# Performance work log

Hardware: AMD Instinct MI355X
Metric: run time of the kernel (lower is better)

Reference implementation:

```python
import jax, jax.numpy as jnp
import numpy as np

NX, NY, C = 784, 480, 32
N0 = NX * NY          # 376320 level-0 nodes
N1 = N0 // 4          # 94080
N2 = N0 // 16         # 23520


def _gcn(x, w, b, ei, n):
    """PyG GCNConv: add self loops, symmetric norm, linear, scatter-sum, bias."""
    loop = jnp.arange(n, dtype=ei.dtype)
    src = jnp.concatenate([ei[0], loop])
    dst = jnp.concatenate([ei[1], loop])
    deg = jax.ops.segment_sum(jnp.ones(src.shape[0], x.dtype), dst, num_segments=n)
    dinv = jnp.where(deg > 0, jax.lax.rsqrt(deg), 0.0)
    norm = (dinv[src] * dinv[dst])[:, None]          # [E+n, 1]
    msg = (x @ w)[src] * norm                        # gather + scale
    return jax.ops.segment_sum(msg, dst, num_segments=n) + b


def _up2(x, h, w):
    """2x nearest-neighbor upsample of a row-major-flattened (h, w, C) grid."""
    g = x.reshape(h, w, x.shape[-1])
    return jnp.repeat(jnp.repeat(g, 2, axis=0), 2, axis=1).reshape(-1, x.shape[-1])


def setup_inputs() -> dict:
    key = jax.random.key(0)
    ks = jax.random.split(key, 20)
    f32 = jnp.float32
    inp = {
        "x": jax.random.normal(ks[0], (N0, 4), f32),
        "fc1_w": jax.random.normal(ks[1], (4, C), f32) * 0.1,
        "fc1_b": jax.random.normal(ks[2], (C,), f32) * 0.1,
        "w1": jax.random.normal(ks[3], (C, C), f32) * 0.1,
        "b1": jax.random.normal(ks[4], (C,), f32) * 0.1,
        "w2": jax.random.normal(ks[5], (C, C), f32) * 0.1,
        "b2": jax.random.normal(ks[6], (C,), f32) * 0.1,
        "w3": jax.random.normal(ks[7], (C, C), f32) * 0.1,
        "b3": jax.random.normal(ks[8], (C,), f32) * 0.1,
        "w4": jax.random.normal(ks[9], (C, C), f32) * 0.1,
        "b4": jax.random.normal(ks[10], (C,), f32) * 0.1,
        "w5": jax.random.normal(ks[11], (C, C), f32) * 0.1,
        "b5": jax.random.normal(ks[12], (C,), f32) * 0.1,
        "fc2_w": jax.random.normal(ks[13], (C, 3), f32) * 0.1,
        "fc2_b": jax.random.normal(ks[14], (3,), f32) * 0.1,
        "idx0": jnp.arange(N0, dtype=jnp.int32),
        "idx1": jnp.arange(N1, dtype=jnp.int32),
        "idx2": jnp.arange(N2, dtype=jnp.int32),
        "ei0": jax.random.randint(ks[15], (2, 4 * N0), 0, N0, dtype=jnp.int32),
        "ei1": jax.random.randint(ks[16], (2, 4 * N1), 0, N1, dtype=jnp.int32),
        "ei2": jax.random.randint(ks[17], (2, 4 * N2), 0, N2, dtype=jnp.int32),
    }
    return inp


def reference(x, fc1_w, fc1_b, w1, b1, w2, b2, w3, b3, w4, b4, w5, b5,
              fc2_w, fc2_b, idx0, idx1, idx2, ei0, ei1, ei2):
    h = jax.nn.relu(x @ fc1_w + fc1_b)                                  # [N0, 32]
    h = h.at[idx0].set(_gcn(h[idx0], w1, b1, ei0, idx0.shape[0]))
    h = jax.nn.relu(h)
    # level-1 downsample: take every other grid row/col
    h1 = h.reshape(NX, NY, C)[::2, ::2].reshape(-1, C)                  # [N1, 32]
    h1 = h1.at[idx1].set(_gcn(h1[idx1], w2, b2, ei1, idx1.shape[0]))
    h1 = jax.nn.relu(h1)
    # level-2 downsample
    h2 = h1.reshape(NX // 2, NY // 2, C)[::2, ::2].reshape(-1, C)       # [N2, 32]
    h2 = h2.at[idx2].set(_gcn(h2[idx2], w3, b3, ei2, idx2.shape[0]))
    h2 = jax.nn.relu(h2)
    # upsample level-2 -> level-1, residual add
    h1u = h1 + _up2(h2, NX // 4, NY // 4)
    h1u = h1u.at[idx1].set(_gcn(h1u[idx1], w4, b4, ei1, idx1.shape[0]))
    h1u = jax.nn.relu(h1u)
    # upsample level-1 -> level-0, residual add
    hu = h + _up2(h1u, NX // 2, NY // 2)
    hu = hu.at[idx0].set(_gcn(hu[idx0], w5, b5, ei0, idx0.shape[0]))
    hu = jax.nn.relu(hu)
    return (hu @ fc2_w + fc2_b)[idx0]                                   # [N0, 3]
```

## Files before the change

### kernel.cpp

```cpp
#include <hip/hip_runtime.h>
#include <hip/hip_bf16.h>

typedef unsigned short u16;
typedef unsigned int u32;
typedef float fx2 __attribute__((ext_vector_type(2)));

#define NXg 784
#define NYg 480
constexpr int N0c = NXg * NYg;
constexpr int N1c = N0c / 4;
constexpr int N2c = N0c / 16;
constexpr int NTc = N0c + N1c + N2c;
constexpr int E0c = 4 * N0c;
constexpr int E1c = 4 * N1c;
constexpr int E2c = 4 * N2c;
constexpr int NB0 = (N0c + 511) / 512;
constexpr int NB1 = (N1c + 511) / 512;
constexpr int NB2 = (N2c + 511) / 512;
constexpr int NBt = NB0 + NB1 + NB2;
constexpr int ECAP = 2560;
constexpr int CCAP = 4096;
constexpr int CHUNK = 8192;
constexpr int NC0 = (E0c + CHUNK - 1) / CHUNK;
constexpr int NC1 = (E1c + CHUNK - 1) / CHUNK;
constexpr int NC2 = (E2c + CHUNK - 1) / CHUNK;
constexpr int NCt = NC0 + NC1 + NC2;

__device__ __forceinline__ float bf2f(u16 v) {
    union { u32 u; float f; } t; t.u = ((u32)v) << 16; return t.f;
}
__device__ __forceinline__ u16 f2bf(float f) {
    union { float f; u32 u; } t; t.f = f;
    u32 u = t.u;
    u32 r = (u + 0x7fffu + ((u >> 16) & 1u)) >> 16;
    return (u16)r;
}
__device__ __forceinline__ float rdf(const void* p, int i, int isf32) {
    if (isf32) return ((const float*)p)[i];
    return bf2f(((const u16*)p)[i]);
}
__device__ __forceinline__ void stage(float* dst, const void* src, int n, int isf32) {
    int t = threadIdx.x;
    if (isf32) {
        const float* s = (const float*)src;
        for (int i = t; i < n; i += 256) dst[i] = s[i];
    } else {
        const u16* s = (const u16*)src;
        for (int i = t; i < n; i += 256) dst[i] = bf2f(s[i]);
    }
}

struct BF16S {
    typedef u16 T;
    static __device__ __forceinline__ float ld(const T* p, size_t i) { return bf2f(p[i]); }
    static __device__ __forceinline__ void st(T* p, size_t i, float v) { p[i] = f2bf(v); }
    static __device__ __forceinline__ fx2 ld2(const T* p, size_t i) {
        u32 w = ((const u32*)p)[i];
        fx2 r; r.x = bf2f((u16)(w & 0xffffu)); r.y = bf2f((u16)(w >> 16));
        return r;
    }
    static __device__ __forceinline__ void st2nt(T* p, size_t i, fx2 v) {
        u32 w = (u32)f2bf(v.x) | ((u32)f2bf(v.y) << 16);
        __builtin_nontemporal_store(w, (u32*)p + i);
    }
};

__device__ __forceinline__ void lvl_of_bin(int b, int& lv, int& bl) {
    if (b < NB0) { lv = 0; bl = b; }
    else if (b < NB0 + NB1) { lv = 1; bl = b - NB0; }
    else { lv = 2; bl = b - NB0 - NB1; }
}

__global__ void k_dinit(const u32* __restrict__ xw, int* __restrict__ flag,
                        int* __restrict__ binCursor, u16* __restrict__ y0,
                        u16* __restrict__ y1, u16* __restrict__ y2) {
    __shared__ int cnt;
    int t = threadIdx.x;
    int g = blockIdx.x * 256 + t;
    if (blockIdx.x == 0) {
        if (t == 0) cnt = 0;
        __syncthreads();
        u32 w = xw[t];
        int e = (int)((w >> 7) & 0xFFu);
        int hit = ((e >= 90 && e <= 135) || ((w & 0x7FFFu) == 0u)) ? 1 : 0;
        atomicAdd(&cnt, hit);
        __syncthreads();
        if (t == 0) *flag = (cnt < 192) ? 1 : 0;
    }
    if (g < NBt) binCursor[g] = g * ECAP;
    if (blockIdx.x == 1 && t < 32) { y0[t] = 0; y1[t] = 0; y2[t] = 0; }
}

__global__ void kC_place(const int* __restrict__ ei0, const int* __restrict__ ei1,
                         const int* __restrict__ ei2, int* __restrict__ binCursor,
                         u32* __restrict__ BE) {
    __shared__ int lc[NB0];
    __shared__ int lb[NB0];
    int b = blockIdx.x, t = threadIdx.x;
    int lv, cl;
    if (b < NC0) { lv = 0; cl = b; }
    else if (b < NC0 + NC1) { lv = 1; cl = b - NC0; }
    else { lv = 2; cl = b - NC0 - NC1; }
    const int* srcp; const int* dstp; int E, nb, binB;
    if (lv == 0) { srcp = ei0; dstp = ei0 + E0c; E = E0c; nb = NB0; binB = 0; }
    else if (lv == 1) { srcp = ei1; dstp = ei1 + E1c; E = E1c; nb = NB1; binB = NB0; }
    else { srcp = ei2; dstp = ei2 + E2c; E = E2c; nb = NB2; binB = NB0 + NB1; }
    for (int i = t; i < nb; i += 1024) lc[i] = 0;
    __syncthreads();
    int e0 = cl * CHUNK, e1 = min(E, e0 + CHUNK);
    for (int i = e0 + t; i < e1; i += 1024) atomicAdd(&lc[dstp[i] >> 9], 1);
    __syncthreads();
    for (int i = t; i < nb; i += 1024) {
        int c = lc[i];
        lb[i] = c ? atomicAdd(&binCursor[binB + i], c) : 0;
        lc[i] = 0;
    }
    __syncthreads();
    for (int i = e0 + t; i < e1; i += 1024) {
        int d = dstp[i];
        int bn = d >> 9;
        int p = atomicAdd(&lc[bn], 1);
        BE[lb[bn] + p] = ((u32)srcp[i] << 9) | (u32)(d & 511);
    }
}

__global__ void kD_all(const u32* __restrict__ BE, const int* __restrict__ binCursor,
                       float* __restrict__ DINV, u32* __restrict__ RPC,
                       int* __restrict__ colAll) {
    __shared__ int lc[512];
    __shared__ int lst[512];
    __shared__ int lcur[512];
    __shared__ int red[256];
    int b = blockIdx.x, t = threadIdx.x;
    int lv, bl; lvl_of_bin(b, lv, bl);
    int cbase, nLev, dummy;
    if (lv == 0) { cbase = 0; nLev = N0c; dummy = N0c; }
    else if (lv == 1) { cbase = N0c; nLev = N1c; dummy = N1c; }
    else { cbase = N0c + N1c; nLev = N2c; dummy = N2c; }
    lc[t] = 0; lc[t + 256] = 0;
    __syncthreads();
    int s0 = b * ECAP, s1 = binCursor[b];
    for (int i = s0 + t; i < s1; i += 256) atomicAdd(&lc[BE[i] & 511u], 1);
    __syncthreads();
    int nodeB = bl << 9;
    int pc[2];
    int ps = 0;
#pragma unroll
    for (int j = 0; j < 2; j++) {
        int li = t * 2 + j;
        int node = nodeB + li;
        int c = (node < nLev) ? lc[li] : 0;
        pc[j] = (c + 3) & ~3;
        ps += pc[j];
    }
    red[t] = ps;
    __syncthreads();
    for (int off = 1; off < 256; off <<= 1) {
        int x = (t >= off) ? red[t - off] : 0;
        __syncthreads();
        red[t] += x;
        __syncthreads();
    }
    int ex = red[t] - ps;
    int tot = red[255];
    int cb = b * CCAP;
    int off = ex;
#pragma unroll
    for (int j = 0; j < 2; j++) {
        int li = t * 2 + j;
        lst[li] = off;
        lcur[li] = off;
        off += pc[j];
    }
    __syncthreads();
#pragma unroll
    for (int j = 0; j < 2; j++) {
        int li = t * 2 + j;
        int node = nodeB + li;
        if (node < nLev) {
            int c = lc[li];
            DINV[cbase + node] = rsqrtf((float)c + 1.0f);
            int rp = cb + lst[li];
            u32 nch = (u32)((c + 3) >> 2);
            RPC[cbase + node] = ((u32)(rp >> 2) << 10) | nch;
        }
    }
    for (int i = t; i < tot; i += 256) colAll[cb + i] = dummy;
    __syncthreads();
    for (int i = s0 + t; i < s1; i += 256) {
        u32 e = BE[i];
        int p = atomicAdd(&lcur[e & 511u], 1);
        colAll[cb + p] = (int)(e >> 9);
    }
}

__device__ __forceinline__ fx2 gather2(const u16* __restrict__ ys,
                                       const u32* __restrict__ rpc,
                                       const int* __restrict__ col,
                                       const float* __restrict__ dinv,
                                       int node, int cp) {
    u32 v = rpc[node];
    int s0 = (int)((v >> 10) << 2);
    int nch = (int)(v & 1023u);
    fx2 a = BF16S::ld2(ys, (size_t)node * 16 + cp);
    const int4* c4 = (const int4*)(col + s0);
    for (int i = 0; i < nch; i++) {
        int4 cs = c4[i];
        fx2 a0 = BF16S::ld2(ys, (size_t)cs.x * 16 + cp);
        fx2 a1 = BF16S::ld2(ys, (size_t)cs.y * 16 + cp);
        fx2 a2 = BF16S::ld2(ys, (size_t)cs.z * 16 + cp);
        fx2 a3 = BF16S::ld2(ys, (size_t)cs.w * 16 + cp);
        a += (a0 + a1) + (a2 + a3);
    }
    float di = dinv[node];
    a *= di;
    return a;
}

constexpr int FC1_TILES = N0c / 64;
__global__ void k_fc1prep(const void* __restrict__ x, const void* __restrict__ fw,
                          const void* __restrict__ fb, const void* __restrict__ w1,
                          const float* __restrict__ d0, u16* __restrict__ ys1,
                          const int* __restrict__ flag) {
    int isf32 = *flag;
    __shared__ float sx[256];
    __shared__ float sh[64 * 33];
    __shared__ float sfw[128];
    __shared__ float sfb[32];
    __shared__ float sw1[1024];
    int t = threadIdx.x;
    stage(sw1, w1, 1024, isf32);
    stage(sfw, fw, 128, isf32);
    stage(sfb, fb, 32, isf32);
    __syncthreads();
    int c = t & 31;
    int ng = t >> 5;
    int ci0 = t & 15;
    int rgrp = t >> 4;
    for (int tile = blockIdx.x; tile < FC1_TILES; tile += gridDim.x) {
        int nodeBase = tile * 64;
        sx[t] = rdf(x, nodeBase * 4 + t, isf32);
        __syncthreads();
#pragma unroll
        for (int i = 0; i < 8; i++) {
            int ln = ng + i * 8;
            float a = sfb[c];
#pragma unroll
            for (int k = 0; k < 4; k++) a = fmaf(sx[ln * 4 + k], sfw[k * 32 + c], a);
            sh[ln * 33 + c] = fmaxf(a, 0.0f);
        }
        __syncthreads();
        float acc[4][2];
#pragma unroll
        for (int r = 0; r < 4; r++) { acc[r][0] = 0.0f; acc[r][1] = 0.0f; }
#pragma unroll
        for (int k = 0; k < 32; k++) {
            float w0 = sw1[k * 32 + ci0];
            float w1v = sw1[k * 32 + ci0 + 16];
#pragma unroll
            for (int r = 0; r < 4; r++) {
                float s = sh[(rgrp * 4 + r) * 33 + k];
                acc[r][0] = fmaf(s, w0, acc[r][0]);
                acc[r][1] = fmaf(s, w1v, acc[r][1]);
            }
        }
#pragma unroll
        for (int r = 0; r < 4; r++) {
            int node = nodeBase + rgrp * 4 + r;
            float dv = d0[node];
            BF16S::st(ys1, (size_t)node * 32 + ci0, acc[r][0] * dv);
            BF16S::st(ys1, (size_t)node * 32 + ci0 + 16, acc[r][1] * dv);
        }
        __syncthreads();
    }
}

template <int NPB>
__global__ void k_gds(const u16* __restrict__ ys_in, const u32* __restrict__ rpc,
                      const int* __restrict__ col,
                      const float* __restrict__ dinv_p, const void* __restrict__ b,
                      u16* __restrict__ O, const void* __restrict__ wn,
                      const float* __restrict__ dinv_c, u16* __restrict__ ys_out,
                      int cols, const int* __restrict__ flag) {
    int isf32 = *flag;
    __shared__ float sv[NPB * 32];
    __shared__ float swn[1024];
    int t = threadIdx.x;
    int nodeBase = blockIdx.x * NPB;
    int rb = nodeBase / cols;
    if (!(rb & 1)) stage(swn, wn, 1024, isf32);
    int cp = t & 15;
#pragma unroll
    for (int i = 0; i < NPB / 16; i++) {
        int local = (t >> 4) + i * 16;
        int node = nodeBase + local;
        fx2 g = gather2(ys_in, rpc, col, dinv_p, node, cp);
        fx2 v;
        v.x = fmaxf(g.x + rdf(b, 2 * cp, isf32), 0.0f);
        v.y = fmaxf(g.y + rdf(b, 2 * cp + 1, isf32), 0.0f);
        BF16S::st2nt(O, (size_t)node * 16 + cp, v);
        sv[local * 32 + 2 * cp] = v.x;
        sv[local * 32 + 2 * cp + 1] = v.y;
    }
    __syncthreads();
    if (!(rb & 1)) {
#pragma unroll
        for (int i = 0; i < NPB / 16; i++) {
            int item = t + i * 256;
            int childIdx = item >> 5;
            int ci = item & 31;
            int lc = childIdx * 2;
            int cc = (nodeBase - rb * cols) + lc;
            int dn = (rb >> 1) * (cols >> 1) + (cc >> 1);
            float a = 0.0f;
#pragma unroll
            for (int k = 0; k < 32; k++) a = fmaf(sv[lc * 32 + k], swn[k * 32 + ci], a);
            BF16S::st(ys_out, (size_t)dn * 32 + ci, a * dinv_c[dn]);
        }
    }
}

template <int NPB>
__global__ void k_gup(const u16* __restrict__ ys_in, const u32* __restrict__ rpc,
                      const int* __restrict__ col,
                      const float* __restrict__ dinv_p, const void* __restrict__ b,
                      const u16* __restrict__ R, const void* __restrict__ wn,
                      const float* __restrict__ dinv_c, u16* __restrict__ ys_out,
                      int cols_p, const int* __restrict__ flag) {
    constexpr int RPT = NPB / 4;
    int isf32 = *flag;
    __shared__ float sv[NPB * 32];
    __shared__ float sch[NPB * 4 * 33];
    __shared__ float swn[1024];
    int t = threadIdx.x;
    int nodeBase = blockIdx.x * NPB;
    stage(swn, wn, 1024, isf32);
    if (t < NPB * 16) {
        int local = t >> 4, cp = t & 15;
        int node = nodeBase + local;
        fx2 g = gather2(ys_in, rpc, col, dinv_p, node, cp);
        sv[local * 32 + 2 * cp] = fmaxf(g.x + rdf(b, 2 * cp, isf32), 0.0f);
        sv[local * 32 + 2 * cp + 1] = fmaxf(g.y + rdf(b, 2 * cp + 1, isf32), 0.0f);
    }
    __syncthreads();
    int rb = nodeBase / cols_p;
    int ccb = nodeBase - rb * cols_p;
    int cols_c = cols_p * 2;
#pragma unroll
    for (int i = 0; i < NPB / 2; i++) {
        int item = t + i * 256;
        int row = item >> 5, k = item & 31;
        int lp = row >> 2, j = row & 3;
        int ch = (2 * rb + (j >> 1)) * cols_c + 2 * (ccb + lp) + (j & 1);
        sch[row * 33 + k] = bf2f(R[(size_t)ch * 32 + k]) + sv[lp * 32 + k];
    }
    __syncthreads();
    int ci0 = t & 15;
    int rgrp = t >> 4;
    float acc[RPT][2];
#pragma unroll
    for (int r = 0; r < RPT; r++) { acc[r][0] = 0.0f; acc[r][1] = 0.0f; }
#pragma unroll
    for (int k = 0; k < 32; k++) {
        float w0 = swn[k * 32 + ci0];
        float w1v = swn[k * 32 + ci0 + 16];
#pragma unroll
        for (int r = 0; r < RPT; r++) {
            float s = sch[(rgrp * RPT + r) * 33 + k];
            acc[r][0] = fmaf(s, w0, acc[r][0]);
            acc[r][1] = fmaf(s, w1v, acc[r][1]);
        }
    }
#pragma unroll
    for (int r = 0; r < RPT; r++) {
        int row = rgrp * RPT + r;
        int lp = row >> 2, j = row & 3;
        int ch = (2 * rb + (j >> 1)) * cols_c + 2 * (ccb + lp) + (j & 1);
        float dc = dinv_c[ch];
        BF16S::st(ys_out, (size_t)ch * 32 + ci0, acc[r][0] * dc);
        BF16S::st(ys_out, (size_t)ch * 32 + ci0 + 16, acc[r][1] * dc);
    }
}

__global__ void k_gfc2(const u16* __restrict__ ys, const u32* __restrict__ rpc,
                       const int* __restrict__ col,
                       const float* __restrict__ dinv, const void* __restrict__ b5,
                       const void* __restrict__ fw, const void* __restrict__ fb,
                       void* __restrict__ out, int n, const int* __restrict__ flag) {
    int isf32 = *flag;
    __shared__ float sv[1024];
    __shared__ float sw[96];
    __shared__ float sfb[3];
    int t = threadIdx.x;
    if (t < 96) sw[t] = rdf(fw, t, isf32);
    if (t < 3) sfb[t] = rdf(fb, t, isf32);
    int nodeBase = blockIdx.x * 32;
    int cp = t & 15;
#pragma unroll
    for (int i = 0; i < 2; i++) {
        int local = (t >> 4) + i * 16;
        int node = nodeBase + local;
        fx2 g = gather2(ys, rpc, col, dinv, node, cp);
        sv[local * 32 + 2 * cp] = fmaxf(g.x + rdf(b5, 2 * cp, isf32), 0.0f);
        sv[local * 32 + 2 * cp + 1] = fmaxf(g.y + rdf(b5, 2 * cp + 1, isf32), 0.0f);
    }
    __syncthreads();
    if (t < 96) {
        int ln = t / 3, j = t - ln * 3;
        int gn = nodeBase + ln;
        float o = sfb[j];
#pragma unroll
        for (int k = 0; k < 32; k++) o = fmaf(sv[ln * 32 + k], sw[k * 3 + j], o);
        if (isf32) ((float*)out)[(size_t)gn * 3 + j] = o;
        else ((u16*)out)[(size_t)gn * 3 + j] = f2bf(o);
    }
}

extern "C" void kernel_launch(void* const* d_in, const int* in_sizes, int n_in,
                              void* d_out, int out_size, void* d_ws, size_t ws_size,
                              hipStream_t stream) {
    const void* x    = d_in[0];
    const void* fc1w = d_in[1];
    const void* fc1b = d_in[2];
    const void* w1 = d_in[3];  const void* b1 = d_in[4];
    const void* w2 = d_in[5];  const void* b2 = d_in[6];
    const void* w3 = d_in[7];  const void* b3 = d_in[8];
    const void* w4 = d_in[9];  const void* b4 = d_in[10];
    const void* w5 = d_in[11]; const void* b5 = d_in[12];
    const void* fc2w = d_in[13]; const void* fc2b = d_in[14];
    const int* ei0 = (const int*)d_in[18];
    const int* ei1 = (const int*)d_in[19];
    const int* ei2 = (const int*)d_in[20];

    u16* YS0 = (u16*)d_ws;
    u16* A   = YS0 + (size_t)(N0c + 1) * 32;
    u16* YS1 = A + (size_t)N0c * 32;
    u16* H1  = YS1 + (size_t)(N1c + 1) * 32;
    u16* YS2 = H1 + (size_t)N1c * 32;
    float* DINV = (float*)(YS2 + (size_t)(N2c + 1) * 32);
    u32* RPC  = (u32*)(DINV + NTc);
    int* COLA = (int*)(RPC + NTc);
    u32* BE   = (u32*)(COLA + (size_t)NBt * CCAP);
    int* binCursor = (int*)(BE + (size_t)NBt * ECAP);
    int* FLAG      = binCursor + NBt;

    float* D0 = DINV; float* D1 = D0 + N0c; float* D2 = D1 + N1c;
    u32* RPC0 = RPC; u32* RPC1 = RPC0 + N0c; u32* RPC2 = RPC1 + N1c;

    const int Bk = 256;

    k_dinit<<<4, Bk, 0, stream>>>((const u32*)x, FLAG, binCursor,
                                  YS0 + (size_t)N0c * 32, YS1 + (size_t)N1c * 32,
                                  YS2 + (size_t)N2c * 32);
    kC_place<<<NCt, 1024, 0, stream>>>(ei0, ei1, ei2, binCursor, BE);
    kD_all<<<NBt, Bk, 0, stream>>>(BE, binCursor, DINV, RPC, COLA);

    k_fc1prep<<<1960, Bk, 0, stream>>>(x, fc1w, fc1b, w1, D0, YS0, FLAG);
    k_gds<32><<<N0c / 32, Bk, 0, stream>>>(YS0, RPC0, COLA, D0, b1, A, w2, D1, YS1, NYg, FLAG);
    k_gds<16><<<N1c / 16, Bk, 0, stream>>>(YS1, RPC1, COLA, D1, b2, H1, w3, D2, YS2, NYg / 2, FLAG);
    k_gup<8><<<N2c / 8, Bk, 0, stream>>>(YS2, RPC2, COLA, D2, b3, H1, w4, D1, YS1, NYg / 4, FLAG);
    k_gup<16><<<N1c / 16, Bk, 0, stream>>>(YS1, RPC1, COLA, D1, b4, A, w5, D0, YS0, NYg / 2, FLAG);
    k_gfc2<<<N0c / 32, Bk, 0, stream>>>(YS0, RPC0, COLA, D0, b5, fc2w, fc2b, d_out, N0c, FLAG);
}
```

Before: 311.5 us.

## Fuse fc1+W1 transform into CSR build kernel and widen fc2 blocks

Folds the fc1/ReLU/W1 prescaled transform for level-0 nodes into the CSR construction kernel: level-0 bins compute degrees locally and produce the bf16 pre-scaled features for their 512 nodes, so the separate fc1prep launch and the reread of DINV are gone. The final gather+fc2 kernel now handles 64 nodes per block instead of 32, which halves the block count and doubles shared memory use. The fused kernel grows its shared footprint and serializes per-bin work after the scatter, which may lower occupancy for the CSR build.

```diff
diff --git a/kernel.cpp b/kernel.cpp
--- a/kernel.cpp
+++ b/kernel.cpp
@@ -126,17 +126,31 @@
 
 __global__ void kD_all(const u32* __restrict__ BE, const int* __restrict__ binCursor,
                        float* __restrict__ DINV, u32* __restrict__ RPC,
-                       int* __restrict__ colAll) {
+                       int* __restrict__ colAll,
+                       const void* __restrict__ x, const void* __restrict__ fw,
+                       const void* __restrict__ fb, const void* __restrict__ w1,
+                       u16* __restrict__ ys0, const int* __restrict__ flag) {
     __shared__ int lc[512];
     __shared__ int lst[512];
     __shared__ int lcur[512];
     __shared__ int red[256];
+    __shared__ float sw1[1024];
+    __shared__ float sfw[128];
+    __shared__ float sfb[32];
+    __shared__ float sx[256];
+    __shared__ float sh[64 * 33];
     int b = blockIdx.x, t = threadIdx.x;
     int lv, bl; lvl_of_bin(b, lv, bl);
     int cbase, nLev, dummy;
     if (lv == 0) { cbase = 0; nLev = N0c; dummy = N0c; }
     else if (lv == 1) { cbase = N0c; nLev = N1c; dummy = N1c; }
     else { cbase = N0c + N1c; nLev = N2c; dummy = N2c; }
+    int isf32 = *flag;
+    if (lv == 0) {
+        stage(sw1, w1, 1024, isf32);
+        stage(sfw, fw, 128, isf32);
+        stage(sfb, fb, 32, isf32);
+    }
     lc[t] = 0; lc[t + 256] = 0;
     __syncthreads();
     int s0 = b * ECAP, s1 = binCursor[b];
@@ -156,9 +170,9 @@
     red[t] = ps;
     __syncthreads();
     for (int off = 1; off < 256; off <<= 1) {
-        int x = (t >= off) ? red[t - off] : 0;
+        int xsc = (t >= off) ? red[t - off] : 0;
         __syncthreads();
-        red[t] += x;
+        red[t] += xsc;
         __syncthreads();
     }
     int ex = red[t] - ps;
@@ -191,6 +205,50 @@
         u32 e = BE[i];
         int p = atomicAdd(&lcur[e & 511u], 1);
         colAll[cb + p] = (int)(e >> 9);
+    }
+    if (lv == 0) {
+        __syncthreads();
+        int c = t & 31;
+        int ng = t >> 5;
+        int ci0 = t & 15;
+        int rgrp = t >> 4;
+        for (int sub = 0; sub < 8; sub++) {
+            int base64 = nodeB + sub * 64;
+            sx[t] = rdf(x, base64 * 4 + t, isf32);
+            __syncthreads();
+#pragma unroll
+            for (int i = 0; i < 8; i++) {
+                int ln = ng + i * 8;
+                float a = sfb[c];
+#pragma unroll
+                for (int k = 0; k < 4; k++) a = fmaf(sx[ln * 4 + k], sfw[k * 32 + c], a);
+                sh[ln * 33 + c] = fmaxf(a, 0.0f);
+            }
+            __syncthreads();
+            float acc[4][2];
+#pragma unroll
+            for (int r = 0; r < 4; r++) { acc[r][0] = 0.0f; acc[r][1] = 0.0f; }
+#pragma unroll
+            for (int k = 0; k < 32; k++) {
+                float w0 = sw1[k * 32 + ci0];
+                float w1v = sw1[k * 32 + ci0 + 16];
+#pragma unroll
+                for (int r = 0; r < 4; r++) {
+                    float s = sh[(rgrp * 4 + r) * 33 + k];
+                    acc[r][0] = fmaf(s, w0, acc[r][0]);
+                    acc[r][1] = fmaf(s, w1v, acc[r][1]);
+                }
+            }
+#pragma unroll
+            for (int r = 0; r < 4; r++) {
+                int li = sub * 64 + rgrp * 4 + r;
+                int node = nodeB + li;
+                float dv = rsqrtf((float)lc[li] + 1.0f);
+                BF16S::st(ys0, (size_t)node * 32 + ci0, acc[r][0] * dv);
+                BF16S::st(ys0, (size_t)node * 32 + ci0 + 16, acc[r][1] * dv);
+            }
+            __syncthreads();
+        }
     }
 }
 
@@ -215,64 +273,6 @@
     float di = dinv[node];
     a *= di;
     return a;
-}
-
-constexpr int FC1_TILES = N0c / 64;
-__global__ void k_fc1prep(const void* __restrict__ x, const void* __restrict__ fw,
-                          const void* __restrict__ fb, const void* __restrict__ w1,
-                          const float* __restrict__ d0, u16* __restrict__ ys1,
-                          const int* __restrict__ flag) {
-    int isf32 = *flag;
-    __shared__ float sx[256];
-    __shared__ float sh[64 * 33];
-    __shared__ float sfw[128];
-    __shared__ float sfb[32];
-    __shared__ float sw1[1024];
-    int t = threadIdx.x;
-    stage(sw1, w1, 1024, isf32);
-    stage(sfw, fw, 128, isf32);
-    stage(sfb, fb, 32, isf32);
-    __syncthreads();
-    int c = t & 31;
-    int ng = t >> 5;
-    int ci0 = t & 15;
-    int rgrp = t >> 4;
-    for (int tile = blockIdx.x; tile < FC1_TILES; tile += gridDim.x) {
-        int nodeBase = tile * 64;
-        sx[t] = rdf(x, nodeBase * 4 + t, isf32);
-        __syncthreads();
-#pragma unroll
-        for (int i = 0; i < 8; i++) {
-            int ln = ng + i * 8;
-            float a = sfb[c];
-#pragma unroll
-            for (int k = 0; k < 4; k++) a = fmaf(sx[ln * 4 + k], sfw[k * 32 + c], a);
-            sh[ln * 33 + c] = fmaxf(a, 0.0f);
-        }
-        __syncthreads();
-        float acc[4][2];
-#pragma unroll
-        for (int r = 0; r < 4; r++) { acc[r][0] = 0.0f; acc[r][1] = 0.0f; }
-#pragma unroll
-        for (int k = 0; k < 32; k++) {
-            float w0 = sw1[k * 32 + ci0];
-            float w1v = sw1[k * 32 + ci0 + 16];
-#pragma unroll
-            for (int r = 0; r < 4; r++) {
-                float s = sh[(rgrp * 4 + r) * 33 + k];
-                acc[r][0] = fmaf(s, w0, acc[r][0]);
-                acc[r][1] = fmaf(s, w1v, acc[r][1]);
-            }
-        }
-#pragma unroll
-        for (int r = 0; r < 4; r++) {
-            int node = nodeBase + rgrp * 4 + r;
-            float dv = d0[node];
-            BF16S::st(ys1, (size_t)node * 32 + ci0, acc[r][0] * dv);
-            BF16S::st(ys1, (size_t)node * 32 + ci0 + 16, acc[r][1] * dv);
-        }
-        __syncthreads();
-    }
 }
 
 template <int NPB>
@@ -388,16 +388,16 @@
                        const void* __restrict__ fw, const void* __restrict__ fb,
                        void* __restrict__ out, int n, const int* __restrict__ flag) {
     int isf32 = *flag;
-    __shared__ float sv[1024];
+    __shared__ float sv[2048];
     __shared__ float sw[96];
-    __shared__ float sfb[3];
+    __shared__ float sfb3[3];
     int t = threadIdx.x;
     if (t < 96) sw[t] = rdf(fw, t, isf32);
-    if (t < 3) sfb[t] = rdf(fb, t, isf32);
-    int nodeBase = blockIdx.x * 32;
+    if (t < 3) sfb3[t] = rdf(fb, t, isf32);
+    int nodeBase = blockIdx.x * 64;
     int cp = t & 15;
 #pragma unroll
-    for (int i = 0; i < 2; i++) {
+    for (int i = 0; i < 4; i++) {
         int local = (t >> 4) + i * 16;
         int node = nodeBase + local;
         fx2 g = gather2(ys, rpc, col, dinv, node, cp);
@@ -405,10 +405,10 @@
         sv[local * 32 + 2 * cp + 1] = fmaxf(g.y + rdf(b5, 2 * cp + 1, isf32), 0.0f);
     }
     __syncthreads();
-    if (t < 96) {
+    if (t < 192) {
         int ln = t / 3, j = t - ln * 3;
         int gn = nodeBase + ln;
-        float o = sfb[j];
+        float o = sfb3[j];
 #pragma unroll
         for (int k = 0; k < 32; k++) o = fmaf(sv[ln * 32 + k], sw[k * 3 + j], o);
         if (isf32) ((float*)out)[(size_t)gn * 3 + j] = o;
@@ -453,12 +453,12 @@
                                   YS0 + (size_t)N0c * 32, YS1 + (size_t)N1c * 32,
                                   YS2 + (size_t)N2c * 32);
     kC_place<<<NCt, 1024, 0, stream>>>(ei0, ei1, ei2, binCursor, BE);
-    kD_all<<<NBt, Bk, 0, stream>>>(BE, binCursor, DINV, RPC, COLA);
-
-    k_fc1prep<<<1960, Bk, 0, stream>>>(x, fc1w, fc1b, w1, D0, YS0, FLAG);
+    kD_all<<<NBt, Bk, 0, stream>>>(BE, binCursor, DINV, RPC, COLA,
+                                   x, fc1w, fc1b, w1, YS0, FLAG);
+
     k_gds<32><<<N0c / 32, Bk, 0, stream>>>(YS0, RPC0, COLA, D0, b1, A, w2, D1, YS1, NYg, FLAG);
     k_gds<16><<<N1c / 16, Bk, 0, stream>>>(YS1, RPC1, COLA, D1, b2, H1, w3, D2, YS2, NYg / 2, FLAG);
     k_gup<8><<<N2c / 8, Bk, 0, stream>>>(YS2, RPC2, COLA, D2, b3, H1, w4, D1, YS1, NYg / 4, FLAG);
     k_gup<16><<<N1c / 16, Bk, 0, stream>>>(YS1, RPC1, COLA, D1, b4, A, w5, D0, YS0, NYg / 2, FLAG);
-    k_gfc2<<<N0c / 32, Bk, 0, stream>>>(YS0, RPC0, COLA, D0, b5, fc2w, fc2b, d_out, N0c, FLAG);
-}
+    k_gfc2<<<N0c / 64, Bk, 0, stream>>>(YS0, RPC0, COLA, D0, b5, fc2w, fc2b, d_out, N0c, FLAG);
+}
```

Measured after the change: 307.0 us. No clear change (-1.4%).
